# Kernel tuning notes

Measured on AMD Instinct MI355X. Metric: run time of the kernel, lower is better.

## Reference

```python
import jax, jax.numpy as jnp
import numpy as np

B, K, D, H, R, MAXP, IMG = 8, 1024, 256, 8, 4, 1024, 224


def _ln(x, g, b, eps=1e-5):
    m = x.mean(-1, keepdims=True)
    v = ((x - m) ** 2).mean(-1, keepdims=True)
    return (x - m) / jnp.sqrt(v + eps) * g + b


def _rope2d(x, coords, cache, image_size):
    b, k, d = x.shape
    half, quarter = d // 2, d // 4
    maxp = cache.shape[0]
    cn = jnp.clip(coords.astype(jnp.float32) / image_size * (maxp - 1), 0, maxp - 1)
    y_idx = cn[..., 0].astype(jnp.int32)
    x_idx = cn[..., 1].astype(jnp.int32)
    yr = cache[y_idx]  # [B,K,quarter,2]
    xr = cache[x_idx]
    xp = x[..., :half].reshape(b, k, quarter, 2)
    yp = x[..., half:].reshape(b, k, quarter, 2)

    def rot(p, r):
        c, s = r[..., 0], r[..., 1]
        p0, p1 = p[..., 0], p[..., 1]
        return jnp.stack([p0 * c - p1 * s, p0 * s + p1 * c], -1).reshape(b, k, half)

    return jnp.concatenate([rot(xp, xr), rot(yp, yr)], -1)


def _mha_zero(xn, Wqkv, bqkv, Wo, bo, key_allowed, num_heads):
    # torch MultiheadAttention with an all-zero token appended to key/value
    # BEFORE projection -> extra key = b_k, extra value = b_v per head.
    b, l, d = xn.shape
    hd = d // num_heads
    Wq, Wk, Wv = jnp.split(Wqkv, 3, axis=0)
    bq, bk, bv = jnp.split(bqkv, 3)
    q = (xn @ Wq.T + bq).reshape(b, l, num_heads, hd)
    k = jnp.concatenate([xn @ Wk.T + bk, jnp.broadcast_to(bk, (b, 1, d))], 1)
    v = jnp.concatenate([xn @ Wv.T + bv, jnp.broadcast_to(bv, (b, 1, d))], 1)
    k = k.reshape(b, l + 1, num_heads, hd)
    v = v.reshape(b, l + 1, num_heads, hd)
    scores = jnp.einsum('bqhd,bkhd->bhqk', q, k) / jnp.sqrt(jnp.float32(hd))
    mask = jnp.concatenate([key_allowed, jnp.ones((b, 1), bool)], 1)  # zero slot always visible
    scores = jnp.where(mask[:, None, None, :], scores, -jnp.inf)
    attn = jax.nn.softmax(scores, axis=-1)
    out = jnp.einsum('bhqk,bkhd->bqhd', attn, v).reshape(b, l, d)
    return out @ Wo.T + bo


def setup_inputs() -> dict:
    key = jax.random.key(0)
    ks = jax.random.split(key, 20)
    x = jax.random.normal(ks[0], (B, K, D), dtype=jnp.float32)
    coords = jax.random.randint(ks[1], (B, K, 2), 0, IMG, dtype=jnp.int32)
    ctx_id_labels = jax.random.randint(ks[2], (B, K), 0, 2, dtype=jnp.int32)
    half = D // 2
    theta = 1.0 / (10000.0 ** (jnp.arange(0, half, 2, dtype=jnp.float32) / half))
    pos = jnp.arange(MAXP, dtype=jnp.float32)
    freqs = pos[:, None] * theta[None, :]
    rope_cache = jnp.stack([jnp.cos(freqs), jnp.sin(freqs)], -1)  # [MAXP, D/4, 2]
    s = 0.02
    return {
        'x': x, 'coords': coords, 'ctx_id_labels': ctx_id_labels,
        'target_embed': s * jax.random.normal(ks[3], (1, 1, D)),
        'context_embed': s * jax.random.normal(ks[4], (1, 1, D)),
        'register_tokens': s * jax.random.normal(ks[5], (1, R, D)),
        'rope_cache': rope_cache,
        'norm_g': jnp.ones((D,)), 'norm_b': jnp.zeros((D,)),
        'ctx_Wqkv': s * jax.random.normal(ks[6], (3 * D, D)),
        'ctx_bqkv': jnp.zeros((3 * D,)),
        'ctx_Wo': s * jax.random.normal(ks[7], (D, D)),
        'ctx_bo': jnp.zeros((D,)),
        'tgt_Wqkv': s * jax.random.normal(ks[8], (3 * D, D)),
        'tgt_bqkv': jnp.zeros((3 * D,)),
        'tgt_Wo': s * jax.random.normal(ks[9], (D, D)),
        'tgt_bo': jnp.zeros((D,)),
        'mlpn_g': jnp.ones((D,)), 'mlpn_b': jnp.zeros((D,)),
        'mlp_W1': s * jax.random.normal(ks[10], (4 * D, D)),
        'mlp_b1': jnp.zeros((4 * D,)),
        'mlp_W2': s * jax.random.normal(ks[11], (D, 4 * D)),
        'mlp_b2': jnp.zeros((D,)),
    }


def reference(x, coords, ctx_id_labels, target_embed, context_embed, register_tokens,
              rope_cache, norm_g, norm_b, ctx_Wqkv, ctx_bqkv, ctx_Wo, ctx_bo,
              tgt_Wqkv, tgt_bqkv, tgt_Wo, tgt_bo, mlpn_g, mlpn_b,
              mlp_W1, mlp_b1, mlp_W2, mlp_b2):
    b, k, d = x.shape
    is_ctx = ctx_id_labels > 0
    x = x + jnp.where(is_ctx[..., None], context_embed, target_embed)
    x = _rope2d(x, coords, rope_cache, IMG)
    registers = register_tokens + context_embed  # [1,R,D]
    x = jnp.concatenate([jnp.broadcast_to(registers, (b, R, d)), x], 1)
    is_ctx_f = jnp.concatenate([jnp.ones((b, R), bool), is_ctx], 1)
    xn = _ln(x, norm_g, norm_b)
    # ctx queries self-attend to context(+zero); tgt queries cross-attend to context(+zero)
    out_ctx = _mha_zero(xn, ctx_Wqkv, ctx_bqkv, ctx_Wo, ctx_bo, is_ctx_f, H)
    out_tgt = _mha_zero(xn, tgt_Wqkv, tgt_bqkv, tgt_Wo, tgt_bo, is_ctx_f, H)
    attn_out = jnp.where(is_ctx_f[..., None], out_ctx, out_tgt)
    attn_out = attn_out[:, R:]
    x = x[:, R:]
    x = x + attn_out
    h = _ln(x, mlpn_g, mlpn_b)
    h = jax.nn.gelu(h @ mlp_W1.T + mlp_b1, approximate=False) @ mlp_W2.T + mlp_b2
    return x + h
```

## Files before the change

kernel.cpp:

```cpp
#include <hip/hip_runtime.h>
#include <stdint.h>
#include <stddef.h>

typedef unsigned short u16;
typedef __bf16 bf16t;
typedef bf16t bf16x8 __attribute__((ext_vector_type(8)));
typedef u16 u16x8 __attribute__((ext_vector_type(8)));
typedef u16 u16x4 __attribute__((ext_vector_type(4)));
typedef float f32x4 __attribute__((ext_vector_type(4)));

__device__ __forceinline__ float bf2f(u16 u) {
  unsigned int x = ((unsigned int)u) << 16;
  return __builtin_bit_cast(float, x);
}
__device__ __forceinline__ u16 f2bf(float f) {
  unsigned int x = __builtin_bit_cast(unsigned int, f);
  x += 0x7fffu + ((x >> 16) & 1u);
  return (u16)(x >> 16);
}
__device__ __forceinline__ u16x8 ld8(const u16* p) { return *(const u16x8*)p; }

__device__ __forceinline__ f32x4 mfma_bf16(u16x8 a, u16x8 b, f32x4 c) {
  return __builtin_amdgcn_mfma_f32_16x16x32_bf16(
      __builtin_bit_cast(bf16x8, a), __builtin_bit_cast(bf16x8, b), c, 0, 0, 0);
}
__device__ __forceinline__ void g2lds16(const u16* g, u16* l) {
  __builtin_amdgcn_global_load_lds(
      (const __attribute__((address_space(1))) unsigned int*)g,
      (__attribute__((address_space(3))) unsigned int*)l, 16, 0, 0);
}
__device__ __forceinline__ void stc(u16* p, float v) { *p = f2bf(v); }
__device__ __forceinline__ void stc(float* p, float v) { *p = v; }

__device__ __forceinline__ float fast_erf(float x) {
  const float ax = fabsf(x);
  const float t = 1.0f / (1.0f + 0.3275911f * ax);
  const float y = 1.0f - (((((1.061405429f * t - 1.453152027f) * t) + 1.421413741f) * t
                  - 0.284496736f) * t + 0.254829592f) * t * __expf(-ax * ax);
  return copysignf(y, x);
}


__global__ __launch_bounds__(256) void cvt_kernel(
    const float* __restrict__ cW, const float* __restrict__ tW,
    const float* __restrict__ cWo_, const float* __restrict__ tWo_,
    const float* __restrict__ W1_, const float* __restrict__ W2_,
    const float* __restrict__ cb, const float* __restrict__ tb,
    u16* __restrict__ wA, u16* __restrict__ wB, u16* __restrict__ woc,
    u16* __restrict__ wot, u16* __restrict__ w1b, u16* __restrict__ w2b,
    float* __restrict__ bA, float* __restrict__ bB,
    const int* __restrict__ labels, int* __restrict__ slotm,
    int* __restrict__ qcnt_c, int* __restrict__ qcnt_t,
    u16* __restrict__ xnc, u16* __restrict__ xnt)
{
  const int blk = blockIdx.x;
  const int tid = threadIdx.x;
  if (blk >= 1026) {
    const int b = blk - 1026;
    const int wave = tid >> 6, lane = tid & 63;
    __shared__ int wcnt[4];
    int base_c = 0, base_t = 0;
    for (int p = 0; p < 4; ++p) {
      const int idx = p * 256 + tid;
      const bool ic = labels[b * 1024 + idx] > 0;
      const unsigned long long mk = __ballot(ic);
      const int lower = __popcll(mk & ((1ull << lane) - 1ull));
      if (lane == 0) wcnt[wave] = __popcll(mk);
      __syncthreads();
      int off = 0, tot = 0;
      #pragma unroll
      for (int i = 0; i < 4; ++i) { if (i < wave) off += wcnt[i]; tot += wcnt[i]; }
      slotm[b * 1024 + idx] = ic ? (base_c + off + lower)
                                 : (base_t + tid - off - lower);
      base_c += tot; base_t += 256 - tot;
      __syncthreads();
    }
    if (tid == 0) { qcnt_c[b] = base_c; qcnt_t[b] = base_t; }
    const int nc4 = base_c + 4;
    const int needA = (nc4 + 127) & ~127;
    const int needB = (base_t + 127) & ~127;
    const u16x8 z8 = {0, 0, 0, 0, 0, 0, 0, 0};
    for (int idx = tid; idx < (needA - nc4) * 32; idx += 256)
      *(u16x8*)&xnc[((size_t)b * 1152 + nc4 + (idx >> 5)) * 256 + (idx & 31) * 8] = z8;
    for (int idx = tid; idx < (needB - base_t) * 32; idx += 256)
      *(u16x8*)&xnt[((size_t)b * 1024 + base_t + (idx >> 5)) * 256 + (idx & 31) * 8] = z8;
    return;
  }
  if (blk >= 1024) {
    const int e = tid * 4;
    if (blk == 1024) {
      #pragma unroll
      for (int j = 0; j < 4; ++j) {
        const int k = e + j;
        bA[k] = (k < 768) ? cb[k] : tb[k - 512];
      }
    } else {
      #pragma unroll
      for (int j = 0; j < 4; ++j) {
        const int k = e + j;
        if (k < 256) bA[1024 + k] = tb[512 + k];
        else if (k < 512) bB[k - 256] = tb[k - 256];
      }
    }
    return;
  }
  const float* s; u16* d;
  if (blk < 192)      { const size_t e = (size_t)blk * 1024; s = cW + e; d = wA + e; }
  else if (blk < 384) { const int lb = blk - 192; const size_t e = (size_t)lb * 1024;
                        s = tW + e; d = (lb < 64) ? (wB + e) : (wA + e + 131072); }
  else if (blk < 448) { const size_t e = (size_t)(blk - 384) * 1024; s = cWo_ + e; d = woc + e; }
  else if (blk < 512) { const size_t e = (size_t)(blk - 448) * 1024; s = tWo_ + e; d = wot + e; }
  else if (blk < 768) { const size_t e = (size_t)(blk - 512) * 1024; s = W1_ + e; d = w1b + e; }
  else                { const size_t e = (size_t)(blk - 768) * 1024; s = W2_ + e; d = w2b + e; }
  const int o = tid * 4;
  const f32x4 v = *(const f32x4*)(s + o);
  u16x4 ov;
  #pragma unroll
  for (int j = 0; j < 4; ++j) ov[j] = f2bf(v[j]);
  *(u16x4*)(d + o) = ov;
}

__global__ __launch_bounds__(256) void prep_kernel(
    const float* __restrict__ x, const int* __restrict__ coords,
    const int* __restrict__ labels, const float* __restrict__ tgt_e,
    const float* __restrict__ ctx_e, const float* __restrict__ regs,
    const float* __restrict__ rope, const float* __restrict__ g,
    const float* __restrict__ bt, const int* __restrict__ slotm,
    float* __restrict__ x0, u16* __restrict__ xnc, u16* __restrict__ xnt)
{
  const int wv = threadIdx.x >> 6, lane = threadIdx.x & 63;
  const int t = blockIdx.x * 4 + wv;
  const int d = lane * 4;
  const int b = t / 1028, l = t - b * 1028;
  f32x4 v;
  u16* dst;
  if (l < 4) {
    const f32x4 rg = *(const f32x4*)&regs[l * 256 + d];
    const f32x4 ce = *(const f32x4*)&ctx_e[d];
    #pragma unroll
    for (int j = 0; j < 4; ++j) v[j] = rg[j] + ce[j];
    dst = &xnc[((size_t)b * 1152 + l) * 256];
  } else {
    const int p = l - 4;
    const bool ic = labels[b * 1024 + p] > 0;
    const float* emb = ic ? ctx_e : tgt_e;
    const int cy = coords[(b * 1024 + p) * 2 + 0];
    const int cx = coords[(b * 1024 + p) * 2 + 1];
    const float fy = fminf(fmaxf(((float)cy / 224.0f) * 1023.0f, 0.0f), 1023.0f);
    const float fx = fminf(fmaxf(((float)cx / 224.0f) * 1023.0f, 0.0f), 1023.0f);
    const int yi = (int)fy, xi = (int)fx;
    const bool second = d >= 128;
    const int ci = second ? yi : xi;
    const int pairi = (d & 127) >> 1;
    const f32x4 rr = *(const f32x4*)&rope[ci * 128 + pairi * 2];
    const int i0 = (second ? 128 : 0) + pairi * 2;
    const size_t base = (size_t)(b * 1024 + p) * 256;
    const f32x4 xv = *(const f32x4*)&x[base + i0];
    const f32x4 ev = *(const f32x4*)&emb[i0];
    const float p0 = xv[0] + ev[0], p1 = xv[1] + ev[1];
    const float p2 = xv[2] + ev[2], p3 = xv[3] + ev[3];
    v[0] = p0 * rr[0] - p1 * rr[1];
    v[1] = p0 * rr[1] + p1 * rr[0];
    v[2] = p2 * rr[2] - p3 * rr[3];
    v[3] = p2 * rr[3] + p3 * rr[2];
    const int rank = slotm[b * 1024 + p];
    dst = ic ? &xnc[((size_t)b * 1152 + 4 + rank) * 256]
             : &xnt[((size_t)b * 1024 + rank) * 256];
  }
  *(f32x4*)&x0[(size_t)t * 256 + d] = v;
  float s1 = v[0] + v[1] + v[2] + v[3];
  #pragma unroll
  for (int off = 1; off < 64; off <<= 1) s1 += __shfl_xor(s1, off);
  const float mean = s1 * (1.0f / 256.0f);
  f32x4 dv;
  float s2 = 0.f;
  #pragma unroll
  for (int j = 0; j < 4; ++j) { dv[j] = v[j] - mean; s2 += dv[j] * dv[j]; }
  #pragma unroll
  for (int off = 1; off < 64; off <<= 1) s2 += __shfl_xor(s2, off);
  const float rstd = rsqrtf(s2 * (1.0f / 256.0f) + 1e-5f);
  const f32x4 gv = *(const f32x4*)&g[d];
  const f32x4 bv = *(const f32x4*)&bt[d];
  u16x4 o;
  #pragma unroll
  for (int j = 0; j < 4; ++j) o[j] = f2bf(dv[j] * rstd * gv[j] + bv[j]);
  *(u16x4*)&dst[d] = o;
}

template <int MI, int EPI, typename CT>
__global__ __launch_bounds__(256) void gemm_bt(
    const u16* __restrict__ A, int lda, const u16* __restrict__ W, int K,
    const float* __restrict__ bias, CT* __restrict__ C, int ldc, int M,
    const float* __restrict__ resid)
{
  constexpr int TM = MI * 32;
  const int mbase = blockIdx.y * TM, nbase = blockIdx.x * 128;
  __shared__ u16 As[TM * 32];
  __shared__ u16 Bs[128 * 32];
  const int tid = threadIdx.x, lane = tid & 63, w = tid >> 6;
  const int quad = lane >> 4, r = lane & 15;
  const int wm = w >> 1, wn = w & 1;
  const int rA = lane >> 2, cA = (lane & 3) * 8;

  f32x4 acc[MI][4];
  #pragma unroll
  for (int i = 0; i < MI; ++i)
    #pragma unroll
    for (int j = 0; j < 4; ++j) acc[i][j] = (f32x4){0.f, 0.f, 0.f, 0.f};

  const int nkt = K >> 5;
  for (int kt = 0; kt < nkt; ++kt) {
    const int k0 = kt * 32;
    #pragma unroll
    for (int j = 0; j < MI / 2; ++j) {
      const int rr = w * (MI * 8) + j * 16;
      g2lds16(&A[(size_t)(mbase + rr + rA) * lda + k0 + cA], &As[rr * 32]);
    }
    #pragma unroll
    for (int j = 0; j < 2; ++j) {
      const int rr = w * 32 + j * 16;
      g2lds16(&W[(size_t)(nbase + rr + rA) * K + k0 + cA], &Bs[rr * 32]);
    }
    __syncthreads();
    u16x8 av[MI], bv[4];
    #pragma unroll
    for (int mi = 0; mi < MI; ++mi) av[mi] = ld8(&As[(wm * (MI * 16) + mi * 16 + r) * 32 + quad * 8]);
    #pragma unroll
    for (int ni = 0; ni < 4; ++ni) bv[ni] = ld8(&Bs[(wn * 64 + ni * 16 + r) * 32 + quad * 8]);
    #pragma unroll
    for (int mi = 0; mi < MI; ++mi)
      #pragma unroll
      for (int ni = 0; ni < 4; ++ni)
        acc[mi][ni] = mfma_bf16(av[mi], bv[ni], acc[mi][ni]);
    __syncthreads();
  }

  #pragma unroll
  for (int mi = 0; mi < MI; ++mi) {
    #pragma unroll
    for (int ni = 0; ni < 4; ++ni) {
      const int col = nbase + wn * 64 + ni * 16 + r;
      const float bs = bias[col];
      const int row0 = mbase + wm * (MI * 16) + mi * 16 + quad * 4;
      #pragma unroll
      for (int i = 0; i < 4; ++i) {
        const int rr2 = row0 + i;
        if (rr2 < M) {
          float v = acc[mi][ni][i] + bs;
          if (EPI == 1) v = 0.5f * v * (1.0f + fast_erf(v * 0.70710678118654752f));
          if (EPI == 2) v += resid[(size_t)rr2 * ldc + col];
          stc(&C[(size_t)rr2 * ldc + col], v);
        }
      }
    }
  }
}

__global__ __launch_bounds__(256) void gemm_qkv(
    const u16* __restrict__ xnc, const u16* __restrict__ xnt,
    const u16* __restrict__ wA, const u16* __restrict__ wB,
    const float* __restrict__ bA, const float* __restrict__ bB,
    u16* __restrict__ qc, u16* __restrict__ qt,
    u16* __restrict__ kbuf, u16* __restrict__ vbufT,
    const int* __restrict__ qcnt_c, const int* __restrict__ qcnt_t)
{
  const int y = blockIdx.y;
  const int nbase = blockIdx.x * 128;
  const u16 *Ap, *Wp; const float* bp;
  int mbase, b;
  bool tgt;
  if (y < 72) {
    tgt = false;
    b = y / 9; const int mt = y - b * 9;
    const int need = (qcnt_c[b] + 4 + 127) & ~127;
    if (mt * 128 >= need) return;
    mbase = b * 1152 + mt * 128;
    Ap = xnc; Wp = wA; bp = bA;
  } else {
    if (nbase >= 256) return;
    tgt = true;
    const int yy = y - 72;
    b = yy >> 3; const int mt = yy & 7;
    const int need = (qcnt_t[b] + 127) & ~127;
    if (mt * 128 >= need) return;
    mbase = b * 1024 + mt * 128;
    Ap = xnt; Wp = wB; bp = bB;
  }

  __shared__ u16 As[128 * 32];
  __shared__ u16 Bs[128 * 32];
  const int tid = threadIdx.x, lane = tid & 63, w = tid >> 6;
  const int quad = lane >> 4, r = lane & 15;
  const int wm = w >> 1, wn = w & 1;
  const int rA = lane >> 2, cA = (lane & 3) * 8;

  f32x4 acc[4][4];
  #pragma unroll
  for (int i = 0; i < 4; ++i)
    #pragma unroll
    for (int j = 0; j < 4; ++j) acc[i][j] = (f32x4){0.f, 0.f, 0.f, 0.f};

  for (int kt = 0; kt < 8; ++kt) {
    const int k0 = kt * 32;
    #pragma unroll
    for (int j = 0; j < 2; ++j) {
      const int rr = w * 32 + j * 16;
      g2lds16(&Ap[(size_t)(mbase + rr + rA) * 256 + k0 + cA], &As[rr * 32]);
      g2lds16(&Wp[(size_t)(nbase + rr + rA) * 256 + k0 + cA], &Bs[rr * 32]);
    }
    __syncthreads();
    u16x8 av[4], bv[4];
    #pragma unroll
    for (int mi = 0; mi < 4; ++mi) av[mi] = ld8(&As[(wm * 64 + mi * 16 + r) * 32 + quad * 8]);
    #pragma unroll
    for (int ni = 0; ni < 4; ++ni) bv[ni] = ld8(&Bs[(wn * 64 + ni * 16 + r) * 32 + quad * 8]);
    #pragma unroll
    for (int mi = 0; mi < 4; ++mi)
      #pragma unroll
      for (int ni = 0; ni < 4; ++ni)
        acc[mi][ni] = mfma_bf16(av[mi], bv[ni], acc[mi][ni]);
    __syncthreads();
  }

  #pragma unroll
  for (int mi = 0; mi < 4; ++mi) {
    #pragma unroll
    for (int ni = 0; ni < 4; ++ni) {
      const int col = nbase + wn * 64 + ni * 16 + r;
      const float bs = bp[col];
      const int row0 = mbase + wm * 64 + mi * 16 + quad * 4;
      if (tgt) {
        #pragma unroll
        for (int i = 0; i < 4; ++i)
          qt[(size_t)(row0 + i) * 256 + col] = f2bf(acc[mi][ni][i] + bs);
      } else if (col < 256) {
        #pragma unroll
        for (int i = 0; i < 4; ++i)
          qc[(size_t)(row0 + i) * 256 + col] = f2bf(acc[mi][ni][i] + bs);
      } else {
        const int slot0 = row0 - b * 1152;
        const int u = col - 256;
        const int z = u >> 9, kv = (u >> 8) & 1, h = (u >> 5) & 7, d = u & 31;
        const size_t zbh = (size_t)(z * 8 + b) * 8 + h;
        if (kv == 0) {
          u16* kp = kbuf + zbh * 36864 + (size_t)slot0 * 32 + d;
          #pragma unroll
          for (int i = 0; i < 4; ++i) kp[i * 32] = f2bf(acc[mi][ni][i] + bs);
        } else {
          u16x4 o;
          #pragma unroll
          for (int i = 0; i < 4; ++i) o[i] = f2bf(acc[mi][ni][i] + bs);
          *(u16x4*)(vbufT + (zbh * 32 + d) * 1152 + slot0) = o;
        }
      }
    }
  }
}

__global__ __launch_bounds__(256) void gemm_wo(
    const u16* __restrict__ Ac, const u16* __restrict__ At,
    const u16* __restrict__ Wc, const u16* __restrict__ Wt,
    const float* __restrict__ bc, const float* __restrict__ btg,
    u16* __restrict__ Cc, u16* __restrict__ Ct,
    const int* __restrict__ cnt_c, const int* __restrict__ cnt_t)
{
  const int z = blockIdx.z;
  const int y = blockIdx.y, b = y >> 4, mt = y & 15;
  const int* bcnt = z ? cnt_t : cnt_c;
  const int need = (bcnt[b] + 63) & ~63;
  if (mt * 64 >= need) return;
  const int mbase = b * 1024 + mt * 64, nbase = blockIdx.x * 128;
  const u16* A = z ? At : Ac;
  const u16* W = z ? Wt : Wc;
  const float* bias = z ? btg : bc;
  u16* C = z ? Ct : Cc;

  __shared__ u16 As[64 * 32];
  __shared__ u16 Bs[128 * 32];
  const int tid = threadIdx.x, lane = tid & 63, w = tid >> 6;
  const int quad = lane >> 4, r = lane & 15;
  const int wm = w >> 1, wn = w & 1;
  const int rA = lane >> 2, cA = (lane & 3) * 8;

  f32x4 acc[2][4];
  #pragma unroll
  for (int i = 0; i < 2; ++i)
    #pragma unroll
    for (int j = 0; j < 4; ++j) acc[i][j] = (f32x4){0.f, 0.f, 0.f, 0.f};

  for (int kt = 0; kt < 8; ++kt) {
    const int k0 = kt * 32;
    g2lds16(&A[(size_t)(mbase + w * 16 + rA) * 256 + k0 + cA], &As[w * 512]);
    #pragma unroll
    for (int j = 0; j < 2; ++j) {
      const int rr = w * 32 + j * 16;
      g2lds16(&W[(size_t)(nbase + rr + rA) * 256 + k0 + cA], &Bs[rr * 32]);
    }
    __syncthreads();
    u16x8 av[2], bv[4];
    #pragma unroll
    for (int mi = 0; mi < 2; ++mi) av[mi] = ld8(&As[(wm * 32 + mi * 16 + r) * 32 + quad * 8]);
    #pragma unroll
    for (int ni = 0; ni < 4; ++ni) bv[ni] = ld8(&Bs[(wn * 64 + ni * 16 + r) * 32 + quad * 8]);
    #pragma unroll
    for (int mi = 0; mi < 2; ++mi)
      #pragma unroll
      for (int ni = 0; ni < 4; ++ni)
        acc[mi][ni] = mfma_bf16(av[mi], bv[ni], acc[mi][ni]);
    __syncthreads();
  }

  #pragma unroll
  for (int mi = 0; mi < 2; ++mi) {
    #pragma unroll
    for (int ni = 0; ni < 4; ++ni) {
      const int col = nbase + wn * 64 + ni * 16 + r;
      const float bs = bias[col];
      const int row0 = mbase + wm * 32 + mi * 16 + quad * 4;
      #pragma unroll
      for (int i = 0; i < 4; ++i)
        C[(size_t)(row0 + i) * 256 + col] = f2bf(acc[mi][ni][i] + bs);
    }
  }
}

__global__ __launch_bounds__(256) void attn4_kernel(
    const u16* __restrict__ qc, const u16* __restrict__ qt,
    const u16* __restrict__ kbuf, const u16* __restrict__ vbufT,
    const float* __restrict__ cbq, const float* __restrict__ tbq,
    const int* __restrict__ qcnt_c, const int* __restrict__ qcnt_t,
    u16* __restrict__ o_c, u16* __restrict__ o_t)
{
  const int qbx = blockIdx.x, h = blockIdx.y, b = blockIdx.z;
  const int nc = qcnt_c[b], nt = qcnt_t[b];
  const int cblk = (nc + 63) >> 6, tblk = (nt + 63) >> 6;
  int z, qsb, qn;
  if (qbx < cblk)            { z = 0; qsb = qbx << 6; qn = nc; }
  else if (qbx - cblk < tblk){ z = 1; qsb = (qbx - cblk) << 6; qn = nt; }
  else return;
  const int nc4 = nc + 4;
  const int ntile = (nc4 + 63) >> 6;
  const float* bq = z ? tbq : cbq;
  const u16* Q = z ? qt : qc;
  u16* obuf = z ? o_t : o_c;
  const int qrow0 = z ? (b * 1024 + qsb) : (b * 1152 + 4 + qsb);

  const int tid = threadIdx.x, lane = tid & 63, w = tid >> 6;
  const int quad = lane >> 4, r = lane & 15;
  const float scale = 0.17677669529663687f;

  __shared__ u16 Ks[2][2048];
  __shared__ u16 Vt[2][32 * 66];
  __shared__ u16 Ps[4][16 * 72];

  const u16x8 qf = ld8(&Q[(size_t)(qrow0 + w * 16 + r) * 256 + h * 32 + quad * 8]);

  float s0 = 0.f;
  #pragma unroll
  for (int j = 0; j < 8; ++j) s0 += bf2f(qf[j]) * bq[256 + h * 32 + quad * 8 + j];
  s0 *= scale;
  s0 += __shfl_xor(s0, 16);
  s0 += __shfl_xor(s0, 32);
  float m_ = s0, l_ = 1.0f;
  f32x4 accA, accB;
  #pragma unroll
  for (int i = 0; i < 4; ++i) {
    accA[i] = bq[512 + h * 32 + quad * 4 + i];
    accB[i] = bq[512 + h * 32 + 16 + quad * 4 + i];
  }

  const size_t zbh = (size_t)(z * 8 + b) * 8 + h;
  const u16* kz = kbuf + zbh * 36864;
  const u16* vz = vbufT + zbh * 36864;
  const int dloc = (w << 3) + (lane >> 3), part = lane & 7;

  g2lds16(&kz[w * 512 + lane * 8], &Ks[0][w * 512]);
  u16x8 vv = ld8(&vz[(size_t)dloc * 1152 + part * 8]);

  for (int t = 0; t < ntile; ++t) {
    const int cur = t & 1, nxt = cur ^ 1;
    #pragma unroll
    for (int j = 0; j < 8; ++j) Vt[cur][dloc * 66 + part * 8 + j] = vv[j];
    __syncthreads();
    if (t + 1 < ntile) {
      g2lds16(&kz[(t + 1) * 2048 + w * 512 + lane * 8], &Ks[nxt][w * 512]);
      vv = ld8(&vz[(size_t)dloc * 1152 + (t + 1) * 64 + part * 8]);
    }

    f32x4 sT[4];
    #pragma unroll
    for (int tt = 0; tt < 4; ++tt) {
      const u16x8 kf = ld8(&Ks[cur][(tt * 16 + r) * 32 + quad * 8]);
      sT[tt] = mfma_bf16(kf, qf, (f32x4){0.f, 0.f, 0.f, 0.f});
    }
    const int kb0 = t * 64 + quad * 4;
    float rm = -3.0e38f;
    float sc[4][4];
    #pragma unroll
    for (int tt = 0; tt < 4; ++tt)
      #pragma unroll
      for (int i = 0; i < 4; ++i) {
        const float kbias = (kb0 + tt * 16 + i < nc4) ? 0.0f : -1e30f;
        sc[tt][i] = sT[tt][i] * scale + kbias;
        rm = fmaxf(rm, sc[tt][i]);
      }
    rm = fmaxf(rm, __shfl_xor(rm, 16));
    rm = fmaxf(rm, __shfl_xor(rm, 32));
    const float mn = fmaxf(m_, rm);
    const float al = __expf(m_ - mn);
    m_ = mn;
    float rs = 0.f;
    u16* ps = &Ps[w][r * 72];
    #pragma unroll
    for (int tt = 0; tt < 4; ++tt) {
      u16x4 pk;
      #pragma unroll
      for (int i = 0; i < 4; ++i) {
        const float pv = __expf(sc[tt][i] - mn);
        rs += pv;
        pk[i] = f2bf(pv);
      }
      *(u16x4*)&ps[tt * 16 + quad * 4] = pk;
    }
    rs += __shfl_xor(rs, 16);
    rs += __shfl_xor(rs, 32);
    l_ = l_ * al + rs;
    #pragma unroll
    for (int i = 0; i < 4; ++i) { accA[i] *= al; accB[i] *= al; }
    #pragma unroll
    for (int kk = 0; kk < 2; ++kk) {
      const u16x8 pf = ld8(&Ps[w][r * 72 + kk * 32 + quad * 8]);
      const u16x8 vf0 = ld8(&Vt[cur][r * 66 + kk * 32 + quad * 8]);
      const u16x8 vf1 = ld8(&Vt[cur][(16 + r) * 66 + kk * 32 + quad * 8]);
      accA = mfma_bf16(vf0, pf, accA);
      accB = mfma_bf16(vf1, pf, accB);
    }
  }

  const int qlocal = qsb + w * 16 + r;
  if (qlocal < qn) {
    const float inv = 1.0f / l_;
    u16x4 oa, ob;
    #pragma unroll
    for (int i = 0; i < 4; ++i) { oa[i] = f2bf(accA[i] * inv); ob[i] = f2bf(accB[i] * inv); }
    const size_t orow = (size_t)b * 1024 + qlocal;
    *(u16x4*)&obuf[orow * 256 + h * 32 + quad * 4] = oa;
    *(u16x4*)&obuf[orow * 256 + h * 32 + 16 + quad * 4] = ob;
  }
}

__global__ __launch_bounds__(256) void select_ln_kernel(
    const float* __restrict__ x0, const u16* __restrict__ po_c,
    const u16* __restrict__ po_t, const int* __restrict__ labels,
    const int* __restrict__ slotm, const float* __restrict__ g,
    const float* __restrict__ bt, float* __restrict__ x1,
    u16* __restrict__ hln)
{
  const int wv = threadIdx.x >> 6, lane = threadIdx.x & 63;
  const int t = blockIdx.x * 4 + wv;
  const int d = lane * 4;
  const int b = t >> 10;
  const size_t row = (size_t)b * 1028 + 4 + (t & 1023);
  const bool ic = labels[t] > 0;
  const u16* po = ic ? po_c : po_t;
  const int slot = slotm[t];
  const f32x4 xv = *(const f32x4*)&x0[row * 256 + d];
  const u16x4 pv = *(const u16x4*)&po[((size_t)b * 1024 + slot) * 256 + d];
  f32x4 v;
  #pragma unroll
  for (int j = 0; j < 4; ++j) v[j] = xv[j] + bf2f(pv[j]);
  *(f32x4*)&x1[(size_t)t * 256 + d] = v;
  float s1 = v[0] + v[1] + v[2] + v[3];
  #pragma unroll
  for (int off = 1; off < 64; off <<= 1) s1 += __shfl_xor(s1, off);
  const float mean = s1 * (1.0f / 256.0f);
  f32x4 dv;
  float s2 = 0.f;
  #pragma unroll
  for (int j = 0; j < 4; ++j) { dv[j] = v[j] - mean; s2 += dv[j] * dv[j]; }
  #pragma unroll
  for (int off = 1; off < 64; off <<= 1) s2 += __shfl_xor(s2, off);
  const float rstd = rsqrtf(s2 * (1.0f / 256.0f) + 1e-5f);
  const f32x4 gv = *(const f32x4*)&g[d];
  const f32x4 bv = *(const f32x4*)&bt[d];
  u16x4 o;
  #pragma unroll
  for (int j = 0; j < 4; ++j) o[j] = f2bf(dv[j] * rstd * gv[j] + bv[j]);
  *(u16x4*)&hln[(size_t)t * 256 + d] = o;
}

extern "C" void kernel_launch(void* const* d_in, const int* in_sizes, int n_in,
                              void* d_out, int out_size, void* d_ws, size_t ws_size,
                              hipStream_t stream) {
  const float* x      = (const float*)d_in[0];
  const int*   coords = (const int*)d_in[1];
  const int*   labels = (const int*)d_in[2];
  const float* tgt_e  = (const float*)d_in[3];
  const float* ctx_e  = (const float*)d_in[4];
  const float* regs   = (const float*)d_in[5];
  const float* rope   = (const float*)d_in[6];
  const float* ng     = (const float*)d_in[7];
  const float* nb     = (const float*)d_in[8];
  const float* cWqkv  = (const float*)d_in[9];
  const float* cbqkv  = (const float*)d_in[10];
  const float* cWo    = (const float*)d_in[11];
  const float* cbo    = (const float*)d_in[12];
  const float* tWqkv  = (const float*)d_in[13];
  const float* tbqkv  = (const float*)d_in[14];
  const float* tWo    = (const float*)d_in[15];
  const float* tbo    = (const float*)d_in[16];
  const float* mg     = (const float*)d_in[17];
  const float* mbeta  = (const float*)d_in[18];
  const float* W1     = (const float*)d_in[19];
  const float* b1     = (const float*)d_in[20];
  const float* W2     = (const float*)d_in[21];
  const float* b2     = (const float*)d_in[22];

  char* ws = (char*)d_ws;
  float* x0     = (float*)(ws + 0);
  u16*   qc     = (u16*)  (ws + 8421376);
  u16*   xnc    = (u16*)  (ws + 13139968);
  u16*   xnt    = (u16*)  (ws + 17858560);
  u16*   qt     = (u16*)  (ws + 22052864);
  u16*   kbuf   = (u16*)  (ws + 26247168);
  u16*   vbufT  = (u16*)  (ws + 35684352);
  u16*   o_c    = (u16*)  (ws + 45121536);
  u16*   o_t    = (u16*)  (ws + 49315840);
  u16*   wA     = (u16*)  (ws + 57704448);
  u16*   wB     = (u16*)  (ws + 58359808);
  u16*   woc    = (u16*)  (ws + 58490880);
  u16*   wot    = (u16*)  (ws + 58621952);
  u16*   w1b    = (u16*)  (ws + 58753024);
  u16*   w2b    = (u16*)  (ws + 59277312);
  float* bA     = (float*)(ws + 59801600);
  float* bB     = (float*)(ws + 59806720);
  int*   slotm  = (int*)  (ws + 59807744);
  int*   qcnt_c = (int*)  (ws + 59840512);
  int*   qcnt_t = (int*)  (ws + 59840544);
  u16*   po_c   = (u16*)  (ws + 8421376);
  u16*   po_t   = (u16*)  (ws + 13139968);
  u16*   hmid   = (u16*)  (ws + 22052864);
  u16*   hln    = (u16*)  (ws + 45121536);
  float* x1     = (float*)(ws + 49315840);

  cvt_kernel<<<dim3(1034), 256, 0, stream>>>(cWqkv, tWqkv, cWo, tWo, W1, W2,
                                             cbqkv, tbqkv,
                                             wA, wB, woc, wot, w1b, w2b, bA, bB,
                                             labels, slotm, qcnt_c, qcnt_t, xnc, xnt);
  prep_kernel<<<dim3(2056), 256, 0, stream>>>(x, coords, labels, tgt_e, ctx_e,
                                              regs, rope, ng, nb, slotm, x0, xnc, xnt);
  gemm_qkv<<<dim3(10, 136), 256, 0, stream>>>(xnc, xnt, wA, wB, bA, bB,
                                              qc, qt, kbuf, vbufT, qcnt_c, qcnt_t);
  attn4_kernel<<<dim3(17, 8, 8), 256, 0, stream>>>(qc, qt, kbuf, vbufT, cbqkv, tbqkv,
                                                   qcnt_c, qcnt_t, o_c, o_t);
  gemm_wo<<<dim3(2, 128, 2), 256, 0, stream>>>(o_c, o_t, woc, wot, cbo, tbo,
                                               po_c, po_t, qcnt_c, qcnt_t);
  select_ln_kernel<<<dim3(2048), 256, 0, stream>>>(x0, po_c, po_t, labels, slotm, mg, mbeta, x1, hln);
  gemm_bt<4, 1, u16><<<dim3(8, 64), 256, 0, stream>>>(hln, 256, w1b, 256, b1, hmid, 1024, 8192, nullptr);
  gemm_bt<2, 2, float><<<dim3(2, 128), 256, 0, stream>>>(hmid, 1024, w2b, 1024, b2, (float*)d_out, 256, 8192, x1);
}
```

Measured before the change: 222.9 us.

## Fuse output projection with residual add, LayerNorm and scatter to token order

The output-projection GEMM now covers the full 256-wide row per block, adds bias and the residual x0, computes the LayerNorm statistics with shuffles and shared memory, and writes x1 and the normalized bf16 activations straight to original token positions through an inverse slot map. The inverse map is built in the label-compaction pass. This drops the separate select/LayerNorm kernel and the bf16 round-trip of the projected outputs. In exchange there are half as many GEMM blocks, more accumulators per thread, and scattered uncoalesced row writes.

```diff
diff --git a/kernel.cpp b/kernel.cpp
--- a/kernel.cpp
+++ b/kernel.cpp
@@ -50,6 +50,7 @@
     u16* __restrict__ wot, u16* __restrict__ w1b, u16* __restrict__ w2b,
     float* __restrict__ bA, float* __restrict__ bB,
     const int* __restrict__ labels, int* __restrict__ slotm,
+    int* __restrict__ inv_c, int* __restrict__ inv_t,
     int* __restrict__ qcnt_c, int* __restrict__ qcnt_t,
     u16* __restrict__ xnc, u16* __restrict__ xnt)
 {
@@ -70,8 +71,15 @@
       int off = 0, tot = 0;
       #pragma unroll
       for (int i = 0; i < 4; ++i) { if (i < wave) off += wcnt[i]; tot += wcnt[i]; }
-      slotm[b * 1024 + idx] = ic ? (base_c + off + lower)
-                                 : (base_t + tid - off - lower);
+      if (ic) {
+        const int rank = base_c + off + lower;
+        slotm[b * 1024 + idx] = rank;
+        inv_c[b * 1024 + rank] = idx;
+      } else {
+        const int rank = base_t + tid - off - lower;
+        slotm[b * 1024 + idx] = rank;
+        inv_t[b * 1024 + rank] = idx;
+      }
       base_c += tot; base_t += 256 - tot;
       __syncthreads();
     }
@@ -357,69 +365,110 @@
   }
 }
 
-__global__ __launch_bounds__(256) void gemm_wo(
+__global__ __launch_bounds__(256) void gemm_wo_fused(
     const u16* __restrict__ Ac, const u16* __restrict__ At,
     const u16* __restrict__ Wc, const u16* __restrict__ Wt,
     const float* __restrict__ bc, const float* __restrict__ btg,
-    u16* __restrict__ Cc, u16* __restrict__ Ct,
-    const int* __restrict__ cnt_c, const int* __restrict__ cnt_t)
+    const int* __restrict__ cnt_c, const int* __restrict__ cnt_t,
+    const int* __restrict__ inv_c, const int* __restrict__ inv_t,
+    const float* __restrict__ x0, const float* __restrict__ g,
+    const float* __restrict__ bt, float* __restrict__ x1,
+    u16* __restrict__ hln)
 {
   const int z = blockIdx.z;
   const int y = blockIdx.y, b = y >> 4, mt = y & 15;
-  const int* bcnt = z ? cnt_t : cnt_c;
-  const int need = (bcnt[b] + 63) & ~63;
-  if (mt * 64 >= need) return;
-  const int mbase = b * 1024 + mt * 64, nbase = blockIdx.x * 128;
+  const int qn = (z ? cnt_t : cnt_c)[b];
+  if (mt * 64 >= ((qn + 63) & ~63)) return;
+  const int mbase = b * 1024 + mt * 64;
   const u16* A = z ? At : Ac;
   const u16* W = z ? Wt : Wc;
   const float* bias = z ? btg : bc;
-  u16* C = z ? Ct : Cc;
+  const int* inv = z ? inv_t : inv_c;
 
   __shared__ u16 As[64 * 32];
-  __shared__ u16 Bs[128 * 32];
+  __shared__ u16 Bs[256 * 32];
+  __shared__ float sums[2][64];
+  __shared__ float sqs[2][64];
   const int tid = threadIdx.x, lane = tid & 63, w = tid >> 6;
   const int quad = lane >> 4, r = lane & 15;
   const int wm = w >> 1, wn = w & 1;
   const int rA = lane >> 2, cA = (lane & 3) * 8;
 
-  f32x4 acc[2][4];
+  f32x4 acc[2][8];
   #pragma unroll
   for (int i = 0; i < 2; ++i)
     #pragma unroll
-    for (int j = 0; j < 4; ++j) acc[i][j] = (f32x4){0.f, 0.f, 0.f, 0.f};
+    for (int j = 0; j < 8; ++j) acc[i][j] = (f32x4){0.f, 0.f, 0.f, 0.f};
 
   for (int kt = 0; kt < 8; ++kt) {
     const int k0 = kt * 32;
     g2lds16(&A[(size_t)(mbase + w * 16 + rA) * 256 + k0 + cA], &As[w * 512]);
     #pragma unroll
-    for (int j = 0; j < 2; ++j) {
-      const int rr = w * 32 + j * 16;
-      g2lds16(&W[(size_t)(nbase + rr + rA) * 256 + k0 + cA], &Bs[rr * 32]);
+    for (int j = 0; j < 4; ++j) {
+      const int rr = w * 64 + j * 16;
+      g2lds16(&W[(size_t)(rr + rA) * 256 + k0 + cA], &Bs[rr * 32]);
     }
     __syncthreads();
-    u16x8 av[2], bv[4];
+    u16x8 av[2], bv[8];
     #pragma unroll
     for (int mi = 0; mi < 2; ++mi) av[mi] = ld8(&As[(wm * 32 + mi * 16 + r) * 32 + quad * 8]);
     #pragma unroll
-    for (int ni = 0; ni < 4; ++ni) bv[ni] = ld8(&Bs[(wn * 64 + ni * 16 + r) * 32 + quad * 8]);
+    for (int ni = 0; ni < 8; ++ni) bv[ni] = ld8(&Bs[(wn * 128 + ni * 16 + r) * 32 + quad * 8]);
     #pragma unroll
     for (int mi = 0; mi < 2; ++mi)
       #pragma unroll
-      for (int ni = 0; ni < 4; ++ni)
+      for (int ni = 0; ni < 8; ++ni)
         acc[mi][ni] = mfma_bf16(av[mi], bv[ni], acc[mi][ni]);
     __syncthreads();
   }
 
+  float biasv[8];
+  #pragma unroll
+  for (int ni = 0; ni < 8; ++ni) biasv[ni] = bias[wn * 128 + ni * 16 + r];
+
   #pragma unroll
   for (int mi = 0; mi < 2; ++mi) {
     #pragma unroll
-    for (int ni = 0; ni < 4; ++ni) {
-      const int col = nbase + wn * 64 + ni * 16 + r;
-      const float bs = bias[col];
-      const int row0 = mbase + wm * 32 + mi * 16 + quad * 4;
-      #pragma unroll
-      for (int i = 0; i < 4; ++i)
-        C[(size_t)(row0 + i) * 256 + col] = f2bf(acc[mi][ni][i] + bs);
+    for (int i = 0; i < 4; ++i) {
+      const int lrow = wm * 32 + mi * 16 + quad * 4 + i;
+      const int slot = mt * 64 + lrow;
+      const int tok = (slot < qn) ? inv[b * 1024 + slot] : 0;
+      const float* x0r = &x0[((size_t)b * 1028 + 4 + tok) * 256];
+      float s = 0.f, sq = 0.f;
+      #pragma unroll
+      for (int ni = 0; ni < 8; ++ni) {
+        const float v = acc[mi][ni][i] + biasv[ni] + x0r[wn * 128 + ni * 16 + r];
+        acc[mi][ni][i] = v;
+        s += v; sq += v * v;
+      }
+      #pragma unroll
+      for (int off = 1; off < 16; off <<= 1) {
+        s += __shfl_xor(s, off);
+        sq += __shfl_xor(sq, off);
+      }
+      if (r == 0) { sums[wn][lrow] = s; sqs[wn][lrow] = sq; }
+    }
+  }
+  __syncthreads();
+  #pragma unroll
+  for (int mi = 0; mi < 2; ++mi) {
+    #pragma unroll
+    for (int i = 0; i < 4; ++i) {
+      const int lrow = wm * 32 + mi * 16 + quad * 4 + i;
+      const int slot = mt * 64 + lrow;
+      if (slot >= qn) continue;
+      const float mean = (sums[0][lrow] + sums[1][lrow]) * (1.0f / 256.0f);
+      const float var = (sqs[0][lrow] + sqs[1][lrow]) * (1.0f / 256.0f) - mean * mean;
+      const float rstd = rsqrtf(var + 1e-5f);
+      const int tok = inv[b * 1024 + slot];
+      const size_t orow = (size_t)b * 1024 + tok;
+      #pragma unroll
+      for (int ni = 0; ni < 8; ++ni) {
+        const int col = wn * 128 + ni * 16 + r;
+        const float v = acc[mi][ni][i];
+        x1[orow * 256 + col] = v;
+        hln[orow * 256 + col] = f2bf((v - mean) * rstd * g[col] + bt[col]);
+      }
     }
   }
 }
@@ -547,46 +596,6 @@
     *(u16x4*)&obuf[orow * 256 + h * 32 + quad * 4] = oa;
     *(u16x4*)&obuf[orow * 256 + h * 32 + 16 + quad * 4] = ob;
   }
-}
-
-__global__ __launch_bounds__(256) void select_ln_kernel(
-    const float* __restrict__ x0, const u16* __restrict__ po_c,
-    const u16* __restrict__ po_t, const int* __restrict__ labels,
-    const int* __restrict__ slotm, const float* __restrict__ g,
-    const float* __restrict__ bt, float* __restrict__ x1,
-    u16* __restrict__ hln)
-{
-  const int wv = threadIdx.x >> 6, lane = threadIdx.x & 63;
-  const int t = blockIdx.x * 4 + wv;
-  const int d = lane * 4;
-  const int b = t >> 10;
-  const size_t row = (size_t)b * 1028 + 4 + (t & 1023);
-  const bool ic = labels[t] > 0;
-  const u16* po = ic ? po_c : po_t;
-  const int slot = slotm[t];
-  const f32x4 xv = *(const f32x4*)&x0[row * 256 + d];
-  const u16x4 pv = *(const u16x4*)&po[((size_t)b * 1024 + slot) * 256 + d];
-  f32x4 v;
-  #pragma unroll
-  for (int j = 0; j < 4; ++j) v[j] = xv[j] + bf2f(pv[j]);
-  *(f32x4*)&x1[(size_t)t * 256 + d] = v;
-  float s1 = v[0] + v[1] + v[2] + v[3];
-  #pragma unroll
-  for (int off = 1; off < 64; off <<= 1) s1 += __shfl_xor(s1, off);
-  const float mean = s1 * (1.0f / 256.0f);
-  f32x4 dv;
-  float s2 = 0.f;
-  #pragma unroll
-  for (int j = 0; j < 4; ++j) { dv[j] = v[j] - mean; s2 += dv[j] * dv[j]; }
-  #pragma unroll
-  for (int off = 1; off < 64; off <<= 1) s2 += __shfl_xor(s2, off);
-  const float rstd = rsqrtf(s2 * (1.0f / 256.0f) + 1e-5f);
-  const f32x4 gv = *(const f32x4*)&g[d];
-  const f32x4 bv = *(const f32x4*)&bt[d];
-  u16x4 o;
-  #pragma unroll
-  for (int j = 0; j < 4; ++j) o[j] = f2bf(dv[j] * rstd * gv[j] + bv[j]);
-  *(u16x4*)&hln[(size_t)t * 256 + d] = o;
 }
 
 extern "C" void kernel_launch(void* const* d_in, const int* in_sizes, int n_in,
@@ -626,36 +635,37 @@
   u16*   vbufT  = (u16*)  (ws + 35684352);
   u16*   o_c    = (u16*)  (ws + 45121536);
   u16*   o_t    = (u16*)  (ws + 49315840);
-  u16*   wA     = (u16*)  (ws + 57704448);
-  u16*   wB     = (u16*)  (ws + 58359808);
-  u16*   woc    = (u16*)  (ws + 58490880);
-  u16*   wot    = (u16*)  (ws + 58621952);
-  u16*   w1b    = (u16*)  (ws + 58753024);
-  u16*   w2b    = (u16*)  (ws + 59277312);
-  float* bA     = (float*)(ws + 59801600);
-  float* bB     = (float*)(ws + 59806720);
-  int*   slotm  = (int*)  (ws + 59807744);
-  int*   qcnt_c = (int*)  (ws + 59840512);
-  int*   qcnt_t = (int*)  (ws + 59840544);
-  u16*   po_c   = (u16*)  (ws + 8421376);
-  u16*   po_t   = (u16*)  (ws + 13139968);
-  u16*   hmid   = (u16*)  (ws + 22052864);
-  u16*   hln    = (u16*)  (ws + 45121536);
-  float* x1     = (float*)(ws + 49315840);
+  u16*   wA     = (u16*)  (ws + 53510144);
+  u16*   wB     = (u16*)  (ws + 54165504);
+  u16*   woc    = (u16*)  (ws + 54296576);
+  u16*   wot    = (u16*)  (ws + 54427648);
+  u16*   w1b    = (u16*)  (ws + 54558720);
+  u16*   w2b    = (u16*)  (ws + 55083008);
+  float* bA     = (float*)(ws + 55607296);
+  float* bB     = (float*)(ws + 55612416);
+  int*   slotm  = (int*)  (ws + 55613440);
+  int*   inv_c  = (int*)  (ws + 55646208);
+  int*   inv_t  = (int*)  (ws + 55678976);
+  int*   qcnt_c = (int*)  (ws + 55711744);
+  int*   qcnt_t = (int*)  (ws + 55711776);
+  u16*   hln    = (u16*)  (ws + 17858560);
+  float* x1     = (float*)(ws + 26247168);
+  u16*   hmid   = (u16*)  (ws + 35684352);
 
   cvt_kernel<<<dim3(1034), 256, 0, stream>>>(cWqkv, tWqkv, cWo, tWo, W1, W2,
                                              cbqkv, tbqkv,
                                              wA, wB, woc, wot, w1b, w2b, bA, bB,
-                                             labels, slotm, qcnt_c, qcnt_t, xnc, xnt);
+                                             labels, slotm, inv_c, inv_t,
+                                             qcnt_c, qcnt_t, xnc, xnt);
   prep_kernel<<<dim3(2056), 256, 0, stream>>>(x, coords, labels, tgt_e, ctx_e,
                                               regs, rope, ng, nb, slotm, x0, xnc, xnt);
   gemm_qkv<<<dim3(10, 136), 256, 0, stream>>>(xnc, xnt, wA, wB, bA, bB,
                                               qc, qt, kbuf, vbufT, qcnt_c, qcnt_t);
   attn4_kernel<<<dim3(17, 8, 8), 256, 0, stream>>>(qc, qt, kbuf, vbufT, cbqkv, tbqkv,
                                                    qcnt_c, qcnt_t, o_c, o_t);
-  gemm_wo<<<dim3(2, 128, 2), 256, 0, stream>>>(o_c, o_t, woc, wot, cbo, tbo,
-                                               po_c, po_t, qcnt_c, qcnt_t);
-  select_ln_kernel<<<dim3(2048), 256, 0, stream>>>(x0, po_c, po_t, labels, slotm, mg, mbeta, x1, hln);
+  gemm_wo_fused<<<dim3(1, 128, 2), 256, 0, stream>>>(o_c, o_t, woc, wot, cbo, tbo,
+                                                     qcnt_c, qcnt_t, inv_c, inv_t,
+                                                     x0, mg, mbeta, x1, hln);
   gemm_bt<4, 1, u16><<<dim3(8, 64), 256, 0, stream>>>(hln, 256, w1b, 256, b1, hmid, 1024, 8192, nullptr);
   gemm_bt<2, 2, float><<<dim3(2, 128), 256, 0, stream>>>(hmid, 1024, w2b, 1024, b2, (float*)d_out, 256, 8192, x1);
 }
```

New measurement: 228.4 us. +2.5%, slower.
